# Kernel optimization log

Hardware: AMD Instinct MI355X
Metric: run time of the kernel (lower is better)

## Reference

```python
import jax, jax.numpy as jnp
import numpy as np

HEAD_SIZE = 64
NUM_HEADS = 16
D_MODEL = HEAD_SIZE * NUM_HEADS  # 1024
B, S = 2, 2048


def setup_inputs() -> dict:
    key = jax.random.key(0)
    ks = jax.random.split(key, 13)
    sc = 1.0 / np.sqrt(D_MODEL)
    inp = {
        'queries': jax.random.normal(ks[0], (B, S, D_MODEL), jnp.float32),
        'keys': jax.random.normal(ks[1], (B, S, D_MODEL), jnp.float32),
        'values': jax.random.normal(ks[2], (B, S, D_MODEL), jnp.float32),
        'mask': jax.random.randint(ks[3], (B, NUM_HEADS, S, S), 0, 2, jnp.int32),
        # nn.Linear weights (out,in) and biases
        'Wq': jax.random.normal(ks[4], (D_MODEL, D_MODEL), jnp.float32) * sc,
        'bq': jax.random.normal(ks[5], (D_MODEL,), jnp.float32) * sc,
        'Wk': jax.random.normal(ks[6], (D_MODEL, D_MODEL), jnp.float32) * sc,
        'bk': jax.random.normal(ks[7], (D_MODEL,), jnp.float32) * sc,
        'Wv': jax.random.normal(ks[8], (D_MODEL, D_MODEL), jnp.float32) * sc,
        'bv': jax.random.normal(ks[9], (D_MODEL,), jnp.float32) * sc,
        'Wy': jax.random.normal(ks[10], (D_MODEL, D_MODEL), jnp.float32) * sc,
        'by': jax.random.normal(ks[11], (D_MODEL,), jnp.float32) * sc,
        # extra nn.Parameter biases (initialized to zeros in the module)
        'bq2': jnp.zeros((D_MODEL,), jnp.float32),
        'bk2': jnp.zeros((D_MODEL,), jnp.float32),
        'bv2': jnp.zeros((D_MODEL,), jnp.float32),
        'by2': jnp.zeros((D_MODEL,), jnp.float32),
    }
    return inp


def _split_heads(x):
    b, s, _ = x.shape
    return x.reshape(b, s, NUM_HEADS, HEAD_SIZE).transpose(0, 2, 1, 3)  # [B,H,S,D]


def _merge_heads(x):
    b, h, s, d = x.shape
    return x.transpose(0, 2, 1, 3).reshape(b, s, h * d)


def mha(queries, keys, values, mask, Wq, bq, bq2, Wk, bk, bk2, Wv, bv, bv2, Wy, by, by2):
    q = queries @ Wq.T + bq + bq2
    k = keys @ Wk.T + bk + bk2
    v = values @ Wv.T + bv + bv2
    q, k, v = _split_heads(q), _split_heads(k), _split_heads(v)  # [B,H,S,D]
    scores = jnp.einsum('bhqd,bhkd->bhqk', q, k) / np.sqrt(HEAD_SIZE).astype(np.float32)
    m = mask.astype(scores.dtype)
    scores = scores * m - 1e4 * (1.0 - m)
    w = jax.nn.softmax(scores, axis=-1)
    out = jnp.einsum('bhqk,bhkd->bhqd', w, v)
    y = _merge_heads(out)  # [B,S,H*D]
    return y @ Wy.T + by + by2


def reference(queries, keys, values, mask, Wq, bq, Wk, bk, Wv, bv, Wy, by, bq2, bk2, bv2, by2):
    return mha(queries, keys, values, mask, Wq, bq, bq2, Wk, bk, bk2, Wv, bv, bv2, Wy, by, by2)
```

## Files before the change

### kernel.cpp

```cpp
#include <hip/hip_runtime.h>
#include <math.h>


typedef _Float16 h8 __attribute__((ext_vector_type(8)));
typedef _Float16 h4 __attribute__((ext_vector_type(4)));
typedef float f4 __attribute__((ext_vector_type(4)));

#define S_LEN 2048
#define DM 1024
#define NH 16
#define HD 64

__global__ __launch_bounds__(256, 2) void qkv_proj_kernel(
    const float* __restrict__ Xq, const float* __restrict__ Xk, const float* __restrict__ Xv,
    const float* __restrict__ Wq, const float* __restrict__ Wk, const float* __restrict__ Wv,
    const float* __restrict__ bq, const float* __restrict__ bk, const float* __restrict__ bv,
    const float* __restrict__ bq2, const float* __restrict__ bk2, const float* __restrict__ bv2,
    _Float16* __restrict__ oq, _Float16* __restrict__ okk, _Float16* __restrict__ ov)
{
    const int z = blockIdx.z;
    const float* X  = (z == 0) ? Xq  : (z == 1) ? Xk  : Xv;
    const float* W  = (z == 0) ? Wq  : (z == 1) ? Wk  : Wv;
    const float* b1 = (z == 0) ? bq  : (z == 1) ? bk  : bv;
    const float* b2 = (z == 0) ? bq2 : (z == 1) ? bk2 : bv2;
    _Float16* outp  = (z == 0) ? oq  : (z == 1) ? okk : ov;

    __shared__ _Float16 As[128][56];
    __shared__ _Float16 Bs[128][56];

    const int tid  = threadIdx.x;
    const int lane = tid & 63;
    const int wave = tid >> 6;
    const int l16  = lane & 15;
    const int g    = lane >> 4;
    const int wm   = (wave >> 1) * 64;
    const int wn   = (wave & 1) * 64;
    const int m0   = blockIdx.x * 128;
    const int n0   = blockIdx.y * 128;

    f4 acc[4][4] = {};

    for (int k0 = 0; k0 < 1024; k0 += 32) {
        __syncthreads();
        #pragma unroll
        for (int r = 0; r < 4; ++r) {
            int f = tid + 256 * r;
            int row = f >> 3;
            int c4  = (f & 7) * 4;
            f4 xa = *(const f4*)(X + (size_t)(m0 + row) * 1024 + k0 + c4);
            f4 xb = *(const f4*)(W + (size_t)(n0 + row) * 1024 + k0 + c4);
            h4 ha = { (_Float16)xa.x, (_Float16)xa.y, (_Float16)xa.z, (_Float16)xa.w };
            h4 hb = { (_Float16)xb.x, (_Float16)xb.y, (_Float16)xb.z, (_Float16)xb.w };
            *(h4*)&As[row][c4] = ha;
            *(h4*)&Bs[row][c4] = hb;
        }
        __syncthreads();

        h8 af[4], bf[4];
        #pragma unroll
        for (int i = 0; i < 4; ++i) af[i] = *(const h8*)&As[wm + i * 16 + l16][g * 8];
        #pragma unroll
        for (int j = 0; j < 4; ++j) bf[j] = *(const h8*)&Bs[wn + j * 16 + l16][g * 8];
        #pragma unroll
        for (int i = 0; i < 4; ++i)
            #pragma unroll
            for (int j = 0; j < 4; ++j)
                acc[i][j] = __builtin_amdgcn_mfma_f32_16x16x32_f16(af[i], bf[j], acc[i][j], 0, 0, 0);
    }

    #pragma unroll
    for (int i = 0; i < 4; ++i)
        #pragma unroll
        for (int j = 0; j < 4; ++j)
            #pragma unroll
            for (int r = 0; r < 4; ++r) {
                int gm = m0 + wm + i * 16 + g * 4 + r;
                int gn = n0 + wn + j * 16 + l16;
                float val = acc[i][j][r] + b1[gn] + b2[gn];
                int b = gm >> 11, s = gm & 2047;
                int h = gn >> 6,  d = gn & 63;
                outp[(((size_t)(b * NH + h) * S_LEN + s) << 6) + d] = (_Float16)val;
            }
}

__global__ __launch_bounds__(256) void transpose_v_kernel(
    const _Float16* __restrict__ v, _Float16* __restrict__ vt)
{
    const int bh = blockIdx.x;
    const int s0 = blockIdx.y * 64;
    __shared__ _Float16 t[64][65];
    const int tid = threadIdx.x;

    #pragma unroll
    for (int r = 0; r < 2; ++r) {
        int u = tid + 256 * r;
        int row = u >> 3, c8 = (u & 7) * 8;
        h8 hv = *(const h8*)(v + ((size_t)bh * S_LEN + s0 + row) * 64 + c8);
        #pragma unroll
        for (int e = 0; e < 8; ++e) t[row][c8 + e] = hv[e];
    }
    __syncthreads();
    #pragma unroll
    for (int r = 0; r < 2; ++r) {
        int u = tid + 256 * r;
        int d = u >> 3, p8 = (u & 7) * 8;
        h8 hv;
        #pragma unroll
        for (int e = 0; e < 8; ++e) {
            int p = p8 + e;
            int c = (p & 3) * 16 + (p >> 2);
            hv[e] = t[c][d];
        }
        *(h8*)(vt + ((size_t)bh * 64 + d) * S_LEN + s0 + p8) = hv;
    }
}

__global__ __launch_bounds__(256, 2) void attn_kernel(
    const _Float16* __restrict__ q_ws, const _Float16* __restrict__ k_ws,
    const _Float16* __restrict__ vt_ws, const int* __restrict__ mask,
    _Float16* __restrict__ o_ws)
{
    const int tid  = threadIdx.x;
    const int lane = tid & 63;
    const int wave = tid >> 6;
    const int g    = lane >> 4;
    const int l16  = lane & 15;
    const int qt   = blockIdx.x;
    const int bh   = blockIdx.y;
    const int q0   = qt * 128;

    __shared__ _Float16 Ks[2][64][72];
    __shared__ _Float16 Vs[2][64][72];
    __shared__ _Float16 Ps[128][72];
    __shared__ unsigned int Ms[2][4][128];

    h8 qf[2][2];
    #pragma unroll
    for (int i = 0; i < 2; ++i)
        #pragma unroll
        for (int ks = 0; ks < 2; ++ks)
            qf[i][ks] = *(const h8*)(q_ws +
                ((size_t)bh * S_LEN + q0 + wave * 32 + i * 16 + l16) * 64 + ks * 32 + g * 8);

    f4 oacc[2][4] = {};
    float lsum[2][4] = {};

    const _Float16* kbase = k_ws + (size_t)bh * S_LEN * 64;
    const _Float16* vbase = vt_ws + (size_t)bh * 64 * S_LEN;
    const int* mbase = mask + ((size_t)bh * S_LEN + q0 + wave * 32) * S_LEN;

    const int srow = tid >> 3;
    const int sc8  = (tid & 7) * 8;

    const float C1 = 0.125f * 1.44269504088896f;
    const float C0 = -5.0f  * 1.44269504088896f;

    {
        h8 k0r[2], v0r[2];
        #pragma unroll
        for (int r = 0; r < 2; ++r) {
            int row = srow + 32 * r;
            k0r[r] = *(const h8*)(kbase + (size_t)row * 64 + sc8);
            v0r[r] = *(const h8*)(vbase + (size_t)row * S_LEN + sc8);
        }
        int4 m0r[8];
        #pragma unroll
        for (int c = 0; c < 8; ++c) {
            int chunk = 64 * c + lane;
            m0r[c] = *(const int4*)(mbase + (size_t)(chunk >> 4) * S_LEN + (chunk & 15) * 4);
        }
        #pragma unroll
        for (int r = 0; r < 2; ++r) {
            int row = srow + 32 * r;
            *(h8*)&Ks[0][row][sc8] = k0r[r];
            *(h8*)&Vs[0][row][sc8] = v0r[r];
        }
        #pragma unroll
        for (int c = 0; c < 8; ++c) {
            int chunk = 64 * c + lane;
            unsigned nib = (unsigned)(m0r[c].x != 0)
                         | ((unsigned)(m0r[c].y != 0) << 1)
                         | ((unsigned)(m0r[c].z != 0) << 2)
                         | ((unsigned)(m0r[c].w != 0) << 3);
            int rr = chunk >> 4, c4 = chunk & 15;
            ((unsigned char*)&Ms[0][wave][0])[rr * 16 + (c4 & 3) * 4 + (c4 >> 2)] =
                (unsigned char)nib;
        }
    }
    __syncthreads();

    for (int kt = 0; kt < 32; ++kt) {
        const int cur = kt & 1;
        const int nxt = cur ^ 1;

        h8 knr[2], vnr[2];
        int4 mnr[8];
        if (kt < 31) {
            const int k1 = (kt + 1) * 64;
            #pragma unroll
            for (int r = 0; r < 2; ++r) {
                int row = srow + 32 * r;
                knr[r] = *(const h8*)(kbase + (size_t)(k1 + row) * 64 + sc8);
                vnr[r] = *(const h8*)(vbase + (size_t)row * S_LEN + k1 + sc8);
            }
            #pragma unroll
            for (int c = 0; c < 8; ++c) {
                int chunk = 64 * c + lane;
                mnr[c] = *(const int4*)(mbase + (size_t)(chunk >> 4) * S_LEN + k1 + (chunk & 15) * 4);
            }
        }

        f4 sacc[2][4] = {};
        #pragma unroll
        for (int ks = 0; ks < 2; ++ks) {
            h8 kf[4];
            #pragma unroll
            for (int j = 0; j < 4; ++j) kf[j] = *(const h8*)&Ks[cur][j * 16 + l16][ks * 32 + g * 8];
            #pragma unroll
            for (int i = 0; i < 2; ++i)
                #pragma unroll
                for (int j = 0; j < 4; ++j)
                    sacc[i][j] = __builtin_amdgcn_mfma_f32_16x16x32_f16(qf[i][ks], kf[j], sacc[i][j], 0, 0, 0);
        }

        #pragma unroll
        for (int i = 0; i < 2; ++i)
            #pragma unroll
            for (int r = 0; r < 4; ++r) {
                int row_local = i * 16 + g * 4 + r;
                unsigned word = Ms[cur][wave][row_local * 4 + (l16 >> 2)];
                unsigned sh = l16 & 3;
                float p0 = ((word >> (sh))      & 1u) ? exp2f(fmaf(sacc[i][0][r], C1, C0)) : 0.0f;
                float p1 = ((word >> (8 + sh))  & 1u) ? exp2f(fmaf(sacc[i][1][r], C1, C0)) : 0.0f;
                float p2 = ((word >> (16 + sh)) & 1u) ? exp2f(fmaf(sacc[i][2][r], C1, C0)) : 0.0f;
                float p3 = ((word >> (24 + sh)) & 1u) ? exp2f(fmaf(sacc[i][3][r], C1, C0)) : 0.0f;
                lsum[i][r] += (p0 + p1) + (p2 + p3);
                h4 ph = { (_Float16)p0, (_Float16)p1, (_Float16)p2, (_Float16)p3 };
                *(h4*)&Ps[wave * 32 + i * 16 + g * 4 + r][l16 * 4] = ph;
            }

        #pragma unroll
        for (int ks = 0; ks < 2; ++ks) {
            h8 pf[2], vf[4];
            #pragma unroll
            for (int i = 0; i < 2; ++i)  pf[i]  = *(const h8*)&Ps[wave * 32 + i * 16 + l16][ks * 32 + g * 8];
            #pragma unroll
            for (int jd = 0; jd < 4; ++jd) vf[jd] = *(const h8*)&Vs[cur][jd * 16 + l16][ks * 32 + g * 8];
            #pragma unroll
            for (int i = 0; i < 2; ++i)
                #pragma unroll
                for (int jd = 0; jd < 4; ++jd)
                    oacc[i][jd] = __builtin_amdgcn_mfma_f32_16x16x32_f16(pf[i], vf[jd], oacc[i][jd], 0, 0, 0);
        }

        if (kt < 31) {
            #pragma unroll
            for (int r = 0; r < 2; ++r) {
                int row = srow + 32 * r;
                *(h8*)&Ks[nxt][row][sc8] = knr[r];
                *(h8*)&Vs[nxt][row][sc8] = vnr[r];
            }
            #pragma unroll
            for (int c = 0; c < 8; ++c) {
                int chunk = 64 * c + lane;
                unsigned nib = (unsigned)(mnr[c].x != 0)
                             | ((unsigned)(mnr[c].y != 0) << 1)
                             | ((unsigned)(mnr[c].z != 0) << 2)
                             | ((unsigned)(mnr[c].w != 0) << 3);
                int rr = chunk >> 4, c4 = chunk & 15;
                ((unsigned char*)&Ms[nxt][wave][0])[rr * 16 + (c4 & 3) * 4 + (c4 >> 2)] =
                    (unsigned char)nib;
            }
        }
        __syncthreads();
    }

    const int b = bh >> 4, h = bh & 15;
    #pragma unroll
    for (int i = 0; i < 2; ++i)
        #pragma unroll
        for (int r = 0; r < 4; ++r) {
            float l = lsum[i][r];
            l += __shfl_xor(l, 1);
            l += __shfl_xor(l, 2);
            l += __shfl_xor(l, 4);
            l += __shfl_xor(l, 8);
            float inv = 1.0f / l;
            int row = q0 + wave * 32 + i * 16 + g * 4 + r;
            #pragma unroll
            for (int jd = 0; jd < 4; ++jd) {
                int d = jd * 16 + l16;
                o_ws[((size_t)b * S_LEN + row) * DM + h * 64 + d] = (_Float16)(oacc[i][jd][r] * inv);
            }
        }
}

__global__ __launch_bounds__(256, 2) void out_proj_kernel(
    const _Float16* __restrict__ A, const float* __restrict__ W,
    const float* __restrict__ b1, const float* __restrict__ b2,
    float* __restrict__ out)
{
    __shared__ _Float16 As[128][56];
    __shared__ _Float16 Bs[128][56];

    const int tid  = threadIdx.x;
    const int lane = tid & 63;
    const int wave = tid >> 6;
    const int l16  = lane & 15;
    const int g    = lane >> 4;
    const int wm   = (wave >> 1) * 64;
    const int wn   = (wave & 1) * 64;
    const int m0   = blockIdx.x * 128;
    const int n0   = blockIdx.y * 128;

    f4 acc[4][4] = {};

    for (int k0 = 0; k0 < 1024; k0 += 32) {
        __syncthreads();
        #pragma unroll
        for (int r = 0; r < 2; ++r) {
            int u = tid + 256 * r;
            int row = u >> 2, c8 = (u & 3) * 8;
            *(h8*)&As[row][c8] = *(const h8*)(A + (size_t)(m0 + row) * 1024 + k0 + c8);
        }
        #pragma unroll
        for (int r = 0; r < 4; ++r) {
            int f = tid + 256 * r;
            int row = f >> 3, c4 = (f & 7) * 4;
            f4 xb = *(const f4*)(W + (size_t)(n0 + row) * 1024 + k0 + c4);
            h4 hb = { (_Float16)xb.x, (_Float16)xb.y, (_Float16)xb.z, (_Float16)xb.w };
            *(h4*)&Bs[row][c4] = hb;
        }
        __syncthreads();

        h8 af[4], bf[4];
        #pragma unroll
        for (int i = 0; i < 4; ++i) af[i] = *(const h8*)&As[wm + i * 16 + l16][g * 8];
        #pragma unroll
        for (int j = 0; j < 4; ++j) bf[j] = *(const h8*)&Bs[wn + j * 16 + l16][g * 8];
        #pragma unroll
        for (int i = 0; i < 4; ++i)
            #pragma unroll
            for (int j = 0; j < 4; ++j)
                acc[i][j] = __builtin_amdgcn_mfma_f32_16x16x32_f16(af[i], bf[j], acc[i][j], 0, 0, 0);
    }

    #pragma unroll
    for (int i = 0; i < 4; ++i)
        #pragma unroll
        for (int j = 0; j < 4; ++j)
            #pragma unroll
            for (int r = 0; r < 4; ++r) {
                int gm = m0 + wm + i * 16 + g * 4 + r;
                int gn = n0 + wn + j * 16 + l16;
                out[(size_t)gm * 1024 + gn] = acc[i][j][r] + b1[gn] + b2[gn];
            }
}

extern "C" void kernel_launch(void* const* d_in, const int* in_sizes, int n_in,
                              void* d_out, int out_size, void* d_ws, size_t ws_size,
                              hipStream_t stream)
{
    (void)in_sizes; (void)n_in; (void)out_size; (void)ws_size;
    const float* queries = (const float*)d_in[0];
    const float* keys    = (const float*)d_in[1];
    const float* values  = (const float*)d_in[2];
    const int*   mask    = (const int*)d_in[3];
    const float* Wq  = (const float*)d_in[4];
    const float* bq  = (const float*)d_in[5];
    const float* Wk  = (const float*)d_in[6];
    const float* bk  = (const float*)d_in[7];
    const float* Wv  = (const float*)d_in[8];
    const float* bv  = (const float*)d_in[9];
    const float* Wy  = (const float*)d_in[10];
    const float* by  = (const float*)d_in[11];
    const float* bq2 = (const float*)d_in[12];
    const float* bk2 = (const float*)d_in[13];
    const float* bv2 = (const float*)d_in[14];
    const float* by2 = (const float*)d_in[15];
    float* out = (float*)d_out;

    char* ws = (char*)d_ws;
    const size_t MB8 = (size_t)8 * 1024 * 1024;
    _Float16* q_ws  = (_Float16*)(ws);
    _Float16* k_ws  = (_Float16*)(ws + 1 * MB8);
    _Float16* v_ws  = (_Float16*)(ws + 2 * MB8);
    _Float16* vt_ws = (_Float16*)(ws + 3 * MB8);
    _Float16* o_ws  = (_Float16*)(ws + 4 * MB8);

    qkv_proj_kernel<<<dim3(32, 8, 3), 256, 0, stream>>>(
        queries, keys, values, Wq, Wk, Wv, bq, bk, bv, bq2, bk2, bv2,
        q_ws, k_ws, v_ws);
    transpose_v_kernel<<<dim3(32, 32), 256, 0, stream>>>(v_ws, vt_ws);
    attn_kernel<<<dim3(16, 32), 256, 0, stream>>>(q_ws, k_ws, vt_ws, mask, o_ws);
    out_proj_kernel<<<dim3(32, 8), 256, 0, stream>>>(o_ws, Wy, by, by2, out);
}
```

Baseline: 870.3 us.

## Pre-convert inputs to fp16 and use direct global-to-LDS loads in projection GEMMs

```diff
diff --git a/kernel.cpp b/kernel.cpp
--- a/kernel.cpp
+++ b/kernel.cpp
@@ -11,22 +11,50 @@
 #define NH 16
 #define HD 64
 
-__global__ __launch_bounds__(256, 2) void qkv_proj_kernel(
-    const float* __restrict__ Xq, const float* __restrict__ Xk, const float* __restrict__ Xv,
-    const float* __restrict__ Wq, const float* __restrict__ Wk, const float* __restrict__ Wv,
+__device__ __forceinline__ void gld16(const void* g, void* l) {
+    __builtin_amdgcn_global_load_lds(
+        (const __attribute__((address_space(1))) void*)g,
+        (__attribute__((address_space(3))) void*)l, 16, 0, 0);
+}
+
+__global__ __launch_bounds__(256) void cvt7_kernel(
+    const float* __restrict__ s0, const float* __restrict__ s1, const float* __restrict__ s2,
+    const float* __restrict__ s3, const float* __restrict__ s4, const float* __restrict__ s5,
+    const float* __restrict__ s6,
+    _Float16* __restrict__ d0, _Float16* __restrict__ d1, _Float16* __restrict__ d2,
+    _Float16* __restrict__ d3, _Float16* __restrict__ d4, _Float16* __restrict__ d5,
+    _Float16* __restrict__ d6)
+{
+    const int z = blockIdx.y;
+    const float* s = (z == 0) ? s0 : (z == 1) ? s1 : (z == 2) ? s2 :
+                     (z == 3) ? s3 : (z == 4) ? s4 : (z == 5) ? s5 : s6;
+    _Float16* d   = (z == 0) ? d0 : (z == 1) ? d1 : (z == 2) ? d2 :
+                     (z == 3) ? d3 : (z == 4) ? d4 : (z == 5) ? d5 : d6;
+    const int n4 = (z < 3) ? (1 << 20) : (1 << 18);
+    const int stride = gridDim.x * 256;
+    for (int i = blockIdx.x * 256 + threadIdx.x; i < n4; i += stride) {
+        f4 v = ((const f4*)s)[i];
+        h4 h = { (_Float16)v.x, (_Float16)v.y, (_Float16)v.z, (_Float16)v.w };
+        ((h4*)d)[i] = h;
+    }
+}
+
+__global__ __launch_bounds__(256, 3) void qkv_proj_kernel(
+    const _Float16* __restrict__ Xq, const _Float16* __restrict__ Xk, const _Float16* __restrict__ Xv,
+    const _Float16* __restrict__ Wqh, const _Float16* __restrict__ Wkh, const _Float16* __restrict__ Wvh,
     const float* __restrict__ bq, const float* __restrict__ bk, const float* __restrict__ bv,
     const float* __restrict__ bq2, const float* __restrict__ bk2, const float* __restrict__ bv2,
     _Float16* __restrict__ oq, _Float16* __restrict__ okk, _Float16* __restrict__ ov)
 {
     const int z = blockIdx.z;
-    const float* X  = (z == 0) ? Xq  : (z == 1) ? Xk  : Xv;
-    const float* W  = (z == 0) ? Wq  : (z == 1) ? Wk  : Wv;
-    const float* b1 = (z == 0) ? bq  : (z == 1) ? bk  : bv;
-    const float* b2 = (z == 0) ? bq2 : (z == 1) ? bk2 : bv2;
-    _Float16* outp  = (z == 0) ? oq  : (z == 1) ? okk : ov;
-
-    __shared__ _Float16 As[128][56];
-    __shared__ _Float16 Bs[128][56];
+    const _Float16* X = (z == 0) ? Xq  : (z == 1) ? Xk  : Xv;
+    const _Float16* W = (z == 0) ? Wqh : (z == 1) ? Wkh : Wvh;
+    const float* b1   = (z == 0) ? bq  : (z == 1) ? bk  : bv;
+    const float* b2   = (z == 0) ? bq2 : (z == 1) ? bk2 : bv2;
+    _Float16* outp    = (z == 0) ? oq  : (z == 1) ? okk : ov;
+
+    __shared__ _Float16 As[128 * 64];
+    __shared__ _Float16 Bs[128 * 64];
 
     const int tid  = threadIdx.x;
     const int lane = tid & 63;
@@ -38,34 +66,49 @@
     const int m0   = blockIdx.x * 128;
     const int n0   = blockIdx.y * 128;
 
+    int rowS[4], colS[4];
+    #pragma unroll
+    for (int c = 0; c < 4; ++c) {
+        int o = wave * 4096 + c * 1024 + lane * 16;
+        int t = o ^ (((o >> 7) & 7) << 4);
+        rowS[c] = t >> 7;
+        colS[c] = (t & 127) >> 1;
+    }
+
     f4 acc[4][4] = {};
 
-    for (int k0 = 0; k0 < 1024; k0 += 32) {
+    for (int k0 = 0; k0 < 1024; k0 += 64) {
         __syncthreads();
         #pragma unroll
-        for (int r = 0; r < 4; ++r) {
-            int f = tid + 256 * r;
-            int row = f >> 3;
-            int c4  = (f & 7) * 4;
-            f4 xa = *(const f4*)(X + (size_t)(m0 + row) * 1024 + k0 + c4);
-            f4 xb = *(const f4*)(W + (size_t)(n0 + row) * 1024 + k0 + c4);
-            h4 ha = { (_Float16)xa.x, (_Float16)xa.y, (_Float16)xa.z, (_Float16)xa.w };
-            h4 hb = { (_Float16)xb.x, (_Float16)xb.y, (_Float16)xb.z, (_Float16)xb.w };
-            *(h4*)&As[row][c4] = ha;
-            *(h4*)&Bs[row][c4] = hb;
+        for (int c = 0; c < 4; ++c) {
+            gld16(X + (size_t)(m0 + rowS[c]) * 1024 + k0 + colS[c],
+                  (char*)As + wave * 4096 + c * 1024);
+            gld16(W + (size_t)(n0 + rowS[c]) * 1024 + k0 + colS[c],
+                  (char*)Bs + wave * 4096 + c * 1024);
         }
         __syncthreads();
 
-        h8 af[4], bf[4];
-        #pragma unroll
-        for (int i = 0; i < 4; ++i) af[i] = *(const h8*)&As[wm + i * 16 + l16][g * 8];
-        #pragma unroll
-        for (int j = 0; j < 4; ++j) bf[j] = *(const h8*)&Bs[wn + j * 16 + l16][g * 8];
-        #pragma unroll
-        for (int i = 0; i < 4; ++i)
-            #pragma unroll
-            for (int j = 0; j < 4; ++j)
-                acc[i][j] = __builtin_amdgcn_mfma_f32_16x16x32_f16(af[i], bf[j], acc[i][j], 0, 0, 0);
+        #pragma unroll
+        for (int ks = 0; ks < 2; ++ks) {
+            h8 af[4], bf[4];
+            #pragma unroll
+            for (int i = 0; i < 4; ++i) {
+                int ra = wm + i * 16 + l16;
+                af[i] = *(const h8*)((const char*)As +
+                        ((ra * 128 + ks * 64 + g * 16) ^ ((l16 & 7) << 4)));
+            }
+            #pragma unroll
+            for (int j = 0; j < 4; ++j) {
+                int rb = wn + j * 16 + l16;
+                bf[j] = *(const h8*)((const char*)Bs +
+                        ((rb * 128 + ks * 64 + g * 16) ^ ((l16 & 7) << 4)));
+            }
+            #pragma unroll
+            for (int i = 0; i < 4; ++i)
+                #pragma unroll
+                for (int j = 0; j < 4; ++j)
+                    acc[i][j] = __builtin_amdgcn_mfma_f32_16x16x32_f16(af[i], bf[j], acc[i][j], 0, 0, 0);
+        }
     }
 
     #pragma unroll
@@ -295,13 +338,13 @@
         }
 }
 
-__global__ __launch_bounds__(256, 2) void out_proj_kernel(
-    const _Float16* __restrict__ A, const float* __restrict__ W,
+__global__ __launch_bounds__(256, 3) void out_proj_kernel(
+    const _Float16* __restrict__ A, const _Float16* __restrict__ W,
     const float* __restrict__ b1, const float* __restrict__ b2,
     float* __restrict__ out)
 {
-    __shared__ _Float16 As[128][56];
-    __shared__ _Float16 Bs[128][56];
+    __shared__ _Float16 As[128 * 64];
+    __shared__ _Float16 Bs[64 * 64];
 
     const int tid  = threadIdx.x;
     const int lane = tid & 63;
@@ -309,46 +352,67 @@
     const int l16  = lane & 15;
     const int g    = lane >> 4;
     const int wm   = (wave >> 1) * 64;
-    const int wn   = (wave & 1) * 64;
+    const int wn   = (wave & 1) * 32;
     const int m0   = blockIdx.x * 128;
-    const int n0   = blockIdx.y * 128;
-
-    f4 acc[4][4] = {};
-
-    for (int k0 = 0; k0 < 1024; k0 += 32) {
+    const int n0   = blockIdx.y * 64;
+
+    int rowA[4], colA[4], rowB[2], colB[2];
+    #pragma unroll
+    for (int c = 0; c < 4; ++c) {
+        int o = wave * 4096 + c * 1024 + lane * 16;
+        int t = o ^ (((o >> 7) & 7) << 4);
+        rowA[c] = t >> 7;
+        colA[c] = (t & 127) >> 1;
+    }
+    #pragma unroll
+    for (int c = 0; c < 2; ++c) {
+        int o = wave * 2048 + c * 1024 + lane * 16;
+        int t = o ^ (((o >> 7) & 7) << 4);
+        rowB[c] = t >> 7;
+        colB[c] = (t & 127) >> 1;
+    }
+
+    f4 acc[4][2] = {};
+
+    for (int k0 = 0; k0 < 1024; k0 += 64) {
         __syncthreads();
         #pragma unroll
-        for (int r = 0; r < 2; ++r) {
-            int u = tid + 256 * r;
-            int row = u >> 2, c8 = (u & 3) * 8;
-            *(h8*)&As[row][c8] = *(const h8*)(A + (size_t)(m0 + row) * 1024 + k0 + c8);
-        }
-        #pragma unroll
-        for (int r = 0; r < 4; ++r) {
-            int f = tid + 256 * r;
-            int row = f >> 3, c4 = (f & 7) * 4;
-            f4 xb = *(const f4*)(W + (size_t)(n0 + row) * 1024 + k0 + c4);
-            h4 hb = { (_Float16)xb.x, (_Float16)xb.y, (_Float16)xb.z, (_Float16)xb.w };
-            *(h4*)&Bs[row][c4] = hb;
-        }
+        for (int c = 0; c < 4; ++c)
+            gld16(A + (size_t)(m0 + rowA[c]) * 1024 + k0 + colA[c],
+                  (char*)As + wave * 4096 + c * 1024);
+        #pragma unroll
+        for (int c = 0; c < 2; ++c)
+            gld16(W + (size_t)(n0 + rowB[c]) * 1024 + k0 + colB[c],
+                  (char*)Bs + wave * 2048 + c * 1024);
         __syncthreads();
 
-        h8 af[4], bf[4];
-        #pragma unroll
-        for (int i = 0; i < 4; ++i) af[i] = *(const h8*)&As[wm + i * 16 + l16][g * 8];
-        #pragma unroll
-        for (int j = 0; j < 4; ++j) bf[j] = *(const h8*)&Bs[wn + j * 16 + l16][g * 8];
-        #pragma unroll
-        for (int i = 0; i < 4; ++i)
-            #pragma unroll
-            for (int j = 0; j < 4; ++j)
-                acc[i][j] = __builtin_amdgcn_mfma_f32_16x16x32_f16(af[i], bf[j], acc[i][j], 0, 0, 0);
+        #pragma unroll
+        for (int ks = 0; ks < 2; ++ks) {
+            h8 af[4], bf[2];
+            #pragma unroll
+            for (int i = 0; i < 4; ++i) {
+                int ra = wm + i * 16 + l16;
+                af[i] = *(const h8*)((const char*)As +
+                        ((ra * 128 + ks * 64 + g * 16) ^ ((l16 & 7) << 4)));
+            }
+            #pragma unroll
+            for (int j = 0; j < 2; ++j) {
+                int rb = wn + j * 16 + l16;
+                bf[j] = *(const h8*)((const char*)Bs +
+                        ((rb * 128 + ks * 64 + g * 16) ^ ((l16 & 7) << 4)));
+            }
+            #pragma unroll
+            for (int i = 0; i < 4; ++i)
+                #pragma unroll
+                for (int j = 0; j < 2; ++j)
+                    acc[i][j] = __builtin_amdgcn_mfma_f32_16x16x32_f16(af[i], bf[j], acc[i][j], 0, 0, 0);
+        }
     }
 
     #pragma unroll
     for (int i = 0; i < 4; ++i)
         #pragma unroll
-        for (int j = 0; j < 4; ++j)
+        for (int j = 0; j < 2; ++j)
             #pragma unroll
             for (int r = 0; r < 4; ++r) {
                 int gm = m0 + wm + i * 16 + g * 4 + r;
@@ -381,17 +445,27 @@
     float* out = (float*)d_out;
 
     char* ws = (char*)d_ws;
-    const size_t MB8 = (size_t)8 * 1024 * 1024;
-    _Float16* q_ws  = (_Float16*)(ws);
-    _Float16* k_ws  = (_Float16*)(ws + 1 * MB8);
-    _Float16* v_ws  = (_Float16*)(ws + 2 * MB8);
-    _Float16* vt_ws = (_Float16*)(ws + 3 * MB8);
-    _Float16* o_ws  = (_Float16*)(ws + 4 * MB8);
-
+    const size_t MB = (size_t)1024 * 1024;
+    _Float16* xq_h  = (_Float16*)(ws +  0 * MB);
+    _Float16* xk_h  = (_Float16*)(ws +  8 * MB);
+    _Float16* xv_h  = (_Float16*)(ws + 16 * MB);
+    _Float16* wq_h  = (_Float16*)(ws + 24 * MB);
+    _Float16* wk_h  = (_Float16*)(ws + 26 * MB);
+    _Float16* wv_h  = (_Float16*)(ws + 28 * MB);
+    _Float16* wy_h  = (_Float16*)(ws + 30 * MB);
+    _Float16* q_ws  = (_Float16*)(ws + 32 * MB);
+    _Float16* k_ws  = (_Float16*)(ws + 40 * MB);
+    _Float16* v_ws  = (_Float16*)(ws + 48 * MB);
+    _Float16* vt_ws = (_Float16*)(ws + 56 * MB);
+    _Float16* o_ws  = (_Float16*)(ws + 64 * MB);
+
+    cvt7_kernel<<<dim3(512, 7), 256, 0, stream>>>(
+        queries, keys, values, Wq, Wk, Wv, Wy,
+        xq_h, xk_h, xv_h, wq_h, wk_h, wv_h, wy_h);
     qkv_proj_kernel<<<dim3(32, 8, 3), 256, 0, stream>>>(
-        queries, keys, values, Wq, Wk, Wv, bq, bk, bv, bq2, bk2, bv2,
-        q_ws, k_ws, v_ws);
+        xq_h, xk_h, xv_h, wq_h, wk_h, wv_h,
+        bq, bk, bv, bq2, bk2, bv2, q_ws, k_ws, v_ws);
     transpose_v_kernel<<<dim3(32, 32), 256, 0, stream>>>(v_ws, vt_ws);
     attn_kernel<<<dim3(16, 32), 256, 0, stream>>>(q_ws, k_ws, vt_ws, mask, o_ws);
-    out_proj_kernel<<<dim3(32, 8), 256, 0, stream>>>(o_ws, Wy, by, by2, out);
-}
+    out_proj_kernel<<<dim3(32, 16), 256, 0, stream>>>(o_ws, wy_h, by, by2, out);
+}
```

After: 835.3 us. 4.0% less time.
